# Performance work log

Measured on AMD Instinct MI355X. Metric: run time of the kernel, lower is better.

## Reference

```python
import jax, jax.numpy as jnp
import numpy as np

BATCH, T, C = 32, 600, 64
DEPTH = 2            # logsig depth 2 -> [increments, Levy areas]
N_SEGMENTS = 50
N_HIDDENS = 512
LOGSIG_CH = C + C * (C - 1) // 2   # 2080, Lyndon-word count at depth 2
IN_SIZE = C + LOGSIG_CH            # 2144 = logsig + start point


def _t_vec(nT, n_segments):
    # matches: [int(round(x)) for x in np.linspace(1, nT, n_segments+1)]
    return np.asarray([int(round(v)) for v in np.linspace(1, nT, n_segments + 1)])


def setup_inputs() -> dict:
    key = jax.random.key(0)
    k0, k1, k2, k3, k4 = jax.random.split(key, 5)
    x = jax.random.normal(k0, (BATCH, T, C), jnp.float32)
    s = 1.0 / np.sqrt(N_HIDDENS)
    w_ih = jax.random.uniform(k1, (4 * N_HIDDENS, IN_SIZE), jnp.float32, -s, s)
    w_hh = jax.random.uniform(k2, (4 * N_HIDDENS, N_HIDDENS), jnp.float32, -s, s)
    b_ih = jax.random.uniform(k3, (4 * N_HIDDENS,), jnp.float32, -s, s)
    b_hh = jax.random.uniform(k4, (4 * N_HIDDENS,), jnp.float32, -s, s)
    return {"x": x, "w_ih": w_ih, "w_hh": w_hh, "b_ih": b_ih, "b_hh": b_hh}


def _logsig_and_start(x):
    """Depth-2 segmented log-signature + segment start points.
    Returns (logsig (B,S,LOGSIG_CH), start (B,S,C))."""
    B, nT, c = x.shape
    tv = _t_vec(nT, N_SEGMENTS)
    starts = tv[:-1] - 1               # segment start frame indices
    ends = tv[1:] - 1                  # segment end frame indices
    # step s (between frames s and s+1) belongs to segment i iff tv[i]-1 <= s < tv[i+1]-1
    step_ids = jnp.asarray(np.searchsorted(tv[1:] - 1, np.arange(nT - 1), side='right'))
    dx = x[:, 1:] - x[:, :-1]                            # (B, T-1, C)
    # per-step outer product x_{t-} (X) dx_t, then segmented sum over steps
    prod = jnp.einsum('btc,btd->btcd', x[:, :-1], dx)    # (B, T-1, C, C)
    Q = jax.ops.segment_sum(jnp.moveaxis(prod, 1, 0), step_ids,
                            num_segments=N_SEGMENTS)      # (S, B, C, C)
    xa = x[:, starts]                                    # (B, S, C)
    xb = x[:, ends]
    inc = xb - xa                                        # level-1 logsig
    # shift origin to segment start: P = sum (X_rel (X) dX)
    P = jnp.moveaxis(Q, 0, 1) - jnp.einsum('bsc,bsd->bscd', xa, inc)
    A = 0.5 * (P - jnp.swapaxes(P, -1, -2))              # Levy area (antisym)
    iu, ju = np.triu_indices(c, 1)                       # Lyndon words (i,j), i<j, lex order
    logsig = jnp.concatenate([inc, A[:, :, iu, ju]], axis=-1)
    return logsig, xa


def _lstm(feats, w_ih, w_hh, b_ih, b_hh):
    B = feats.shape[0]
    H = N_HIDDENS
    gx = jnp.einsum('bsf,gf->bsg', feats, w_ih) + b_ih + b_hh  # (B,S,4H)

    def step(carry, g_t):
        h, cc = carry
        g = g_t + h @ w_hh.T
        i, f, gg, o = jnp.split(g, 4, axis=-1)
        i = jax.nn.sigmoid(i); f = jax.nn.sigmoid(f)
        gg = jnp.tanh(gg); o = jax.nn.sigmoid(o)
        cc = f * cc + i * gg
        h = o * jnp.tanh(cc)
        return (h, cc), h

    h0 = jnp.zeros((B, H), feats.dtype)
    (_, _), hs = jax.lax.scan(step, (h0, h0), jnp.moveaxis(gx, 1, 0))
    return jnp.moveaxis(hs, 0, 1)                        # (B, S, H)


def reference(x, w_ih, w_hh, b_ih, b_hh):
    logsig, x_sp = _logsig_and_start(x)
    feats = jnp.concatenate([logsig, x_sp], axis=-1)      # (B, S, IN_SIZE)
    return _lstm(feats, w_ih, w_hh, b_ih, b_hh)
```

## Files before the change

kernel.cpp:

```cpp
#include <hip/hip_runtime.h>
#include <math.h>

typedef _Float16 f16;
typedef _Float16 f16x8 __attribute__((ext_vector_type(8)));
typedef _Float16 f16x4 __attribute__((ext_vector_type(4)));
typedef float    f32x4 __attribute__((ext_vector_type(4)));

#define BATCH 32
#define TT    600
#define CC    64
#define SEG   50
#define HH    512
#define G4    2048
#define FF    2144
#define MM    1600
#define MP    1664
#define NPAIR 2016
#define CVB   512
#define WRK   208
#define SLOT16 16384

struct TV { int v[51]; };

__device__ __forceinline__ void async_copy16(char* lds, const char* g) {
  __builtin_amdgcn_global_load_lds(
      (const __attribute__((address_space(1))) unsigned int*)g,
      (__attribute__((address_space(3))) unsigned int*)lds, 16, 0, 0);
}

__device__ __forceinline__ float sigm(float x) { return 1.f / (1.f + __expf(-x)); }
__device__ __forceinline__ float tanh_(float x) {
  float ax = fabsf(x);
  float e  = __expf(2.f * ax);
  float t  = 1.f - 2.f / (e + 1.f);
  return x < 0.f ? -t : t;
}
__device__ __forceinline__ unsigned short f16_bits(f16 v) {
  union { f16 f; unsigned short u; } c; c.f = v; return c.u;
}
__device__ __forceinline__ unsigned int f32_bits(float v) {
  union { float f; unsigned int u; } c; c.f = v; return c.u;
}

__global__ void prep_kernel(const float* __restrict__ x, f16* __restrict__ fhi, TV tv,
                            const float4* __restrict__ w_ih, const float4* __restrict__ w_hh,
                            f16x4* __restrict__ w16, f16x4* __restrict__ whh16,
                            unsigned int* __restrict__ ready) {
  __shared__ float xs[13 * CC];
  int m   = blockIdx.x;
  int tid = threadIdx.x;

  if (m >= MP) {
    int cb   = m - MP;
    int gtid = cb * 256 + tid;
    int nth  = CVB * 256;
    for (int i = gtid; i < G4 * FF / 4; i += nth) {
      float4 v = w_ih[i];
      f16x4 o = {(f16)v.x, (f16)v.y, (f16)v.z, (f16)v.w};
      w16[i] = o;
    }
    for (int i = gtid; i < G4 * HH / 4; i += nth) {
      float4 v = w_hh[i];
      f16x4 o = {(f16)v.x, (f16)v.y, (f16)v.z, (f16)v.w};
      whh16[i] = o;
    }
    if (cb == 0)
      for (int i = tid; i < 544; i += 256) ready[i] = 0u;
    return;
  }

  f16* rhi = fhi + (size_t)m * FF;
  if (m >= MM) {
    unsigned int* a = (unsigned int*)rhi;
    for (int i = tid; i < FF / 2; i += 256) a[i] = 0u;
    return;
  }
  int bb = m & 31, ss = m >> 5;
  int t0 = tv.v[ss] - 1, t1 = tv.v[ss + 1] - 1;
  int len = t1 - t0;
  for (int i = tid; i < (len + 1) * CC; i += 256)
    xs[i] = x[(size_t)bb * TT * CC + (size_t)(t0 + (i >> 6)) * CC + (i & 63)];
  __syncthreads();

  if (tid < CC) {
    float xa  = xs[tid];
    float inc = xs[len * CC + tid] - xa;
    rhi[tid] = (f16)inc;
    rhi[2080 + tid] = (f16)xa;
  }

  int p0 = tid * 8;
  if (p0 < NPAIR) {
    int c = 0, rem = p0;
    while (rem >= 63 - c) { rem -= 63 - c; c++; }
    int d = c + 1 + rem;
    int cs[8], dd[8];
#pragma unroll
    for (int i = 0; i < 8; i++) {
      cs[i] = c; dd[i] = d;
      d++; if (d == 64) { c++; d = c + 1; }
    }
    float acc[8], xc[8], xd[8];
#pragma unroll
    for (int i = 0; i < 8; i++) { acc[i] = 0.f; xc[i] = xs[cs[i]]; xd[i] = xs[dd[i]]; }
    for (int t = 1; t <= len; t++) {
#pragma unroll
      for (int i = 0; i < 8; i++) {
        float nc = xs[t * CC + cs[i]], nd = xs[t * CC + dd[i]];
        acc[i] += xc[i] * (nd - xd[i]) - xd[i] * (nc - xc[i]);
        xc[i] = nc; xd[i] = nd;
      }
    }
#pragma unroll
    for (int i = 0; i < 8; i++) {
      int ci = cs[i], di = dd[i];
      float xac = xs[ci], xad = xs[di];
      float incc = xs[len * CC + ci] - xac, incd = xs[len * CC + di] - xad;
      float v = 0.5f * acc[i] - 0.5f * (xac * incd - xad * incc);
      rhi[64 + p0 + i] = (f16)v;
    }
  }
}

__global__ __launch_bounds__(256) void fused_kernel(
    const f16* __restrict__ fhi, const f16* __restrict__ w16,
    const float* __restrict__ bih, const float* __restrict__ bhh,
    const f16* __restrict__ whh16, float* __restrict__ gx,
    unsigned short* __restrict__ hbuf, unsigned int* __restrict__ ready,
    unsigned int* __restrict__ gxcnt, float* __restrict__ out) {
  __shared__ __align__(16) char smem[40960];
  int tid  = threadIdx.x;
  int lane = tid & 63;

  if (blockIdx.x >= 32) {
    int w  = blockIdx.x - 32;
    int wn = tid >> 6;
    char* ldsA = smem;
    char* ldsB = smem + 4096;
    int rowq = tid >> 2;
    int colq = (tid & 3) * 8;
    int ldst = tid * 16;
    int quad16 = (lane >> 4) * 16;
    int am = lane & 15;
    unsigned int* gxa = (unsigned int*)gx;

    for (int t = 0; t < 2; t++) {
      int id = w + t * WRK;
      int mt = id >> 4, nt = id & 15;
      int m0 = mt * 64, n0 = nt * 128;

      const f16* pa  = fhi + (size_t)(m0 + rowq) * FF + colq;
      const f16* pb0 = w16 + (size_t)(n0 + rowq) * FF + colq;
      const f16* pb1 = pb0 + (size_t)64 * FF;

      f32x4 zero4 = {0.f, 0.f, 0.f, 0.f};
      f32x4 acc[4][2];
#pragma unroll
      for (int i = 0; i < 4; i++) { acc[i][0] = zero4; acc[i][1] = zero4; }

      for (int kt = 0; kt < FF / 32; kt++) {
        int koff = kt * 32;
        async_copy16(ldsA + ldst,        (const char*)(pa + koff));
        async_copy16(ldsB + ldst,        (const char*)(pb0 + koff));
        async_copy16(ldsB + 4096 + ldst, (const char*)(pb1 + koff));
        __syncthreads();

        f16x8 bfr[2];
#pragma unroll
        for (int ni = 0; ni < 2; ni++)
          bfr[ni] = *(const f16x8*)(ldsB + (wn * 32 + ni * 16 + am) * 64 + quad16);
#pragma unroll
        for (int mi = 0; mi < 4; mi++) {
          f16x8 ah = *(const f16x8*)(ldsA + (mi * 16 + am) * 64 + quad16);
#pragma unroll
          for (int ni = 0; ni < 2; ni++)
            acc[mi][ni] = __builtin_amdgcn_mfma_f32_16x16x32_f16(ah, bfr[ni], acc[mi][ni], 0, 0, 0);
        }
        __syncthreads();
      }

#pragma unroll
      for (int ni = 0; ni < 2; ni++) {
        int ncol = n0 + wn * 32 + ni * 16 + (lane & 15);
        float bv = bih[ncol] + bhh[ncol];
#pragma unroll
        for (int mi = 0; mi < 4; mi++) {
          int mrow = m0 + mi * 16 + (lane >> 4) * 4;
#pragma unroll
          for (int r = 0; r < 4; r++)
            __hip_atomic_store(gxa + (size_t)(mrow + r) * G4 + ncol,
                               f32_bits(acc[mi][ni][r] + bv),
                               __ATOMIC_RELAXED, __HIP_MEMORY_SCOPE_AGENT);
        }
      }
      __syncthreads();
      if (tid == 0)
        __hip_atomic_fetch_add(&gxcnt[mt], 1u, __ATOMIC_RELAXED,
                               __HIP_MEMORY_SCOPE_AGENT);
    }
    return;
  }

  f16* hs = (f16*)smem;
  float* gb = (float*)(smem + 32768);

  int gate = tid >> 6;
  int u0   = blockIdx.x * 16;
  int wg   = blockIdx.x;

  f16x8 bf[16];
  {
    const f16* wrow = whh16 + (size_t)(gate * HH + u0 + (lane & 15)) * HH + (lane >> 4) * 8;
#pragma unroll
    for (int ks = 0; ks < 16; ks++) bf[ks] = *(const f16x8*)(wrow + ks * 32);
  }

  int b1 = tid >> 4;
  int ul = tid & 15;
  float cst0 = 0.f, cst1 = 0.f;
  int aq  = (lane >> 4);
  int am  = (lane & 15);
  int col = lane & 15;
  int rbase = (lane >> 4) * 4;

  for (int s = 0; s < SEG; s++) {
    if ((s & 1) == 0) {
      if (tid == 0) {
        while (__hip_atomic_load(&gxcnt[s >> 1], __ATOMIC_RELAXED,
                                 __HIP_MEMORY_SCOPE_AGENT) < 16u)
          __builtin_amdgcn_s_sleep(1);
      }
      __syncthreads();
    }

    float gxr0[4], gxr1[4];
#pragma unroll
    for (int r = 0; r < 4; r++) {
      int b = rbase + r;
      gxr0[r] = gx[(size_t)((s << 5) + b) * G4 + gate * HH + u0 + col];
      gxr1[r] = gx[(size_t)((s << 5) + b + 16) * G4 + gate * HH + u0 + col];
    }

    f32x4 acc0 = {0.f, 0.f, 0.f, 0.f};
    f32x4 acc1 = {0.f, 0.f, 0.f, 0.f};

    if (s > 0) {
      unsigned int tgt = (unsigned int)s;
      if (tid < 32) {
        while (__hip_atomic_load(&ready[tid * 16], __ATOMIC_RELAXED,
                                 __HIP_MEMORY_SCOPE_AGENT) < tgt)
          __builtin_amdgcn_s_sleep(1);
      }
      __syncthreads();

      const char* hrd = (const char*)(hbuf + (size_t)s * SLOT16);
#pragma unroll
      for (int c = 0; c < 8; c++)
        async_copy16((char*)hs + c * 4096 + tid * 16, hrd + c * 4096 + tid * 16);
      __syncthreads();

#pragma unroll
      for (int ks = 0; ks < 16; ks++) {
        f16x8 a0 = *(const f16x8*)((char*)hs + (((ks * 4 + aq) * 32) + am) * 16);
        f16x8 a1 = *(const f16x8*)((char*)hs + (((ks * 4 + aq) * 32) + 16 + am) * 16);
        acc0 = __builtin_amdgcn_mfma_f32_16x16x32_f16(a0, bf[ks], acc0, 0, 0, 0);
        acc1 = __builtin_amdgcn_mfma_f32_16x16x32_f16(a1, bf[ks], acc1, 0, 0, 0);
      }
    }

#pragma unroll
    for (int r = 0; r < 4; r++) {
      int b = rbase + r;
      gb[(gate * 32 + b) * 16 + col]      = acc0[r] + gxr0[r];
      gb[(gate * 32 + b + 16) * 16 + col] = acc1[r] + gxr1[r];
    }
    __syncthreads();

    unsigned short* hwr = hbuf + (size_t)(s + 1) * SLOT16;
    int k = u0 + ul;
    float h0, h1;
    {
      float i_ = sigm(gb[(0 * 32 + b1) * 16 + ul]), f_ = sigm(gb[(1 * 32 + b1) * 16 + ul]);
      float g_ = tanh_(gb[(2 * 32 + b1) * 16 + ul]), o_ = sigm(gb[(3 * 32 + b1) * 16 + ul]);
      cst0 = f_ * cst0 + i_ * g_;
      h0 = o_ * tanh_(cst0);
      out[(size_t)(b1 * SEG + s) * HH + k] = h0;
    }
    {
      int b2 = b1 + 16;
      float i_ = sigm(gb[(0 * 32 + b2) * 16 + ul]), f_ = sigm(gb[(1 * 32 + b2) * 16 + ul]);
      float g_ = tanh_(gb[(2 * 32 + b2) * 16 + ul]), o_ = sigm(gb[(3 * 32 + b2) * 16 + ul]);
      cst1 = f_ * cst1 + i_ * g_;
      h1 = o_ * tanh_(cst1);
      out[(size_t)(b2 * SEG + s) * HH + k] = h1;
    }

    if (s < SEG - 1) {
      __hip_atomic_store(hwr + ((k >> 3) * 32 + b1) * 8 + (k & 7),
                         f16_bits((f16)h0), __ATOMIC_RELAXED, __HIP_MEMORY_SCOPE_AGENT);
      __hip_atomic_store(hwr + ((k >> 3) * 32 + (b1 + 16)) * 8 + (k & 7),
                         f16_bits((f16)h1), __ATOMIC_RELAXED, __HIP_MEMORY_SCOPE_AGENT);
      __syncthreads();
      if (tid == 0)
        __hip_atomic_store(&ready[wg * 16], (unsigned int)(s + 1),
                           __ATOMIC_RELAXED, __HIP_MEMORY_SCOPE_AGENT);
    }
  }
}

extern "C" void kernel_launch(void* const* d_in, const int* in_sizes, int n_in,
                              void* d_out, int out_size, void* d_ws, size_t ws_size,
                              hipStream_t stream) {
  const float* x    = (const float*)d_in[0];
  const float* w_ih = (const float*)d_in[1];
  const float* w_hh = (const float*)d_in[2];
  const float* b_ih = (const float*)d_in[3];
  const float* b_hh = (const float*)d_in[4];
  float* out = (float*)d_out;

  char* ws = (char*)d_ws;
  f16*   fhi   = (f16*)(ws + 0);
  f16*   w16   = (f16*)(ws + 7135232);
  f16*   whh16 = (f16*)(ws + 15921152);
  float* gx    = (float*)(ws + 18018304);
  unsigned short* hbuf  = (unsigned short*)(ws + 31649792);
  unsigned int*   ready = (unsigned int*)(ws + 33288192);

  TV tv;
  double step = 599.0 / 50.0;
  for (int i = 0; i <= 50; i++) {
    double v = (double)i * step + 1.0;
    tv.v[i] = (int)nearbyint(v);
  }
  tv.v[50] = 600;

  unsigned int* gxcnt = ready + 512;

  prep_kernel<<<dim3(MP + CVB), dim3(256), 0, stream>>>(
      x, fhi, tv, (const float4*)w_ih, (const float4*)w_hh,
      (f16x4*)w16, (f16x4*)whh16, ready);

  fused_kernel<<<dim3(32 + WRK), dim3(256), 0, stream>>>(
      fhi, w16, b_ih, b_hh, whh16, gx, hbuf, ready, gxcnt, out);
}
```

Before: 264.8 us.

## Pack LSTM recurrence flags, poll per wave, prefetch two steps of gx

Ready flags drop their 16-word padding and sit in consecutive words. Each wave polls them itself, lane-distributed, instead of tid<32 spinning followed by a block barrier. The gx values for two timesteps are loaded after each gxcnt wait, and the elementwise cell update now gives each thread two adjacent units of one batch row, so hidden state is stored as packed 32-bit f16 pairs and outputs as float2. The aim is fewer barriers and narrow atomic stores on the serial recurrence path. The cost is packed flags that may share cache lines and more register pressure.

Result: slower. 274.7 us (+3.8%).

```diff
diff --git a/kernel.cpp b/kernel.cpp
--- a/kernel.cpp
+++ b/kernel.cpp
@@ -35,8 +35,8 @@
   float t  = 1.f - 2.f / (e + 1.f);
   return x < 0.f ? -t : t;
 }
-__device__ __forceinline__ unsigned short f16_bits(f16 v) {
-  union { f16 f; unsigned short u; } c; c.f = v; return c.u;
+__device__ __forceinline__ unsigned int f16_bits(f16 v) {
+  union { f16 f; unsigned short u; } c; c.f = v; return (unsigned int)c.u;
 }
 __device__ __forceinline__ unsigned int f32_bits(float v) {
   union { float f; unsigned int u; } c; c.f = v; return c.u;
@@ -65,7 +65,7 @@
       whh16[i] = o;
     }
     if (cb == 0)
-      for (int i = tid; i < 544; i += 256) ready[i] = 0u;
+      if (tid < 64) ready[tid] = 0u;
     return;
   }
 
@@ -205,6 +205,7 @@
   float* gb = (float*)(smem + 32768);
 
   int gate = tid >> 6;
+  int wave = gate;
   int u0   = blockIdx.x * 16;
   int wg   = blockIdx.x;
 
@@ -215,44 +216,40 @@
     for (int ks = 0; ks < 16; ks++) bf[ks] = *(const f16x8*)(wrow + ks * 32);
   }
 
-  int b1 = tid >> 4;
-  int ul = tid & 15;
-  float cst0 = 0.f, cst1 = 0.f;
   int aq  = (lane >> 4);
   int am  = (lane & 15);
   int col = lane & 15;
   int rbase = (lane >> 4) * 4;
+  int ub = tid >> 3;
+  int uj = tid & 7;
+  int koct = (u0 >> 3) + (uj >> 2);
+  float cstA = 0.f, cstB = 0.f;
+  int pollp = ((lane & 7) << 2) | wave;
+
+  float gxA[2][4], gxB[2][4];
 
   for (int s = 0; s < SEG; s++) {
-    if ((s & 1) == 0) {
-      if (tid == 0) {
-        while (__hip_atomic_load(&gxcnt[s >> 1], __ATOMIC_RELAXED,
-                                 __HIP_MEMORY_SCOPE_AGENT) < 16u)
-          __builtin_amdgcn_s_sleep(1);
-      }
-      __syncthreads();
-    }
-
-    float gxr0[4], gxr1[4];
-#pragma unroll
-    for (int r = 0; r < 4; r++) {
-      int b = rbase + r;
-      gxr0[r] = gx[(size_t)((s << 5) + b) * G4 + gate * HH + u0 + col];
-      gxr1[r] = gx[(size_t)((s << 5) + b + 16) * G4 + gate * HH + u0 + col];
+    if (!(s & 1)) {
+      while (__hip_atomic_load(&gxcnt[s >> 1], __ATOMIC_RELAXED,
+                               __HIP_MEMORY_SCOPE_AGENT) < 16u)
+        __builtin_amdgcn_s_sleep(1);
+#pragma unroll
+      for (int h = 0; h < 2; h++)
+#pragma unroll
+        for (int r = 0; r < 4; r++) {
+          int b = rbase + r;
+          gxA[h][r] = gx[(size_t)(((s + h) << 5) + b) * G4 + gate * HH + u0 + col];
+          gxB[h][r] = gx[(size_t)(((s + h) << 5) + b + 16) * G4 + gate * HH + u0 + col];
+        }
     }
 
     f32x4 acc0 = {0.f, 0.f, 0.f, 0.f};
     f32x4 acc1 = {0.f, 0.f, 0.f, 0.f};
 
     if (s > 0) {
-      unsigned int tgt = (unsigned int)s;
-      if (tid < 32) {
-        while (__hip_atomic_load(&ready[tid * 16], __ATOMIC_RELAXED,
-                                 __HIP_MEMORY_SCOPE_AGENT) < tgt)
-          __builtin_amdgcn_s_sleep(1);
-      }
-      __syncthreads();
-
+      while (__hip_atomic_load(&ready[pollp], __ATOMIC_RELAXED,
+                               __HIP_MEMORY_SCOPE_AGENT) < (unsigned int)s)
+        __builtin_amdgcn_s_sleep(1);
       const char* hrd = (const char*)(hbuf + (size_t)s * SLOT16);
 #pragma unroll
       for (int c = 0; c < 8; c++)
@@ -268,43 +265,36 @@
       }
     }
 
+    int hsel = s & 1;
 #pragma unroll
     for (int r = 0; r < 4; r++) {
       int b = rbase + r;
-      gb[(gate * 32 + b) * 16 + col]      = acc0[r] + gxr0[r];
-      gb[(gate * 32 + b + 16) * 16 + col] = acc1[r] + gxr1[r];
+      gb[(gate * 32 + b) * 16 + col]      = acc0[r] + gxA[hsel][r];
+      gb[(gate * 32 + b + 16) * 16 + col] = acc1[r] + gxB[hsel][r];
     }
     __syncthreads();
 
-    unsigned short* hwr = hbuf + (size_t)(s + 1) * SLOT16;
-    int k = u0 + ul;
-    float h0, h1;
-    {
-      float i_ = sigm(gb[(0 * 32 + b1) * 16 + ul]), f_ = sigm(gb[(1 * 32 + b1) * 16 + ul]);
-      float g_ = tanh_(gb[(2 * 32 + b1) * 16 + ul]), o_ = sigm(gb[(3 * 32 + b1) * 16 + ul]);
-      cst0 = f_ * cst0 + i_ * g_;
-      h0 = o_ * tanh_(cst0);
-      out[(size_t)(b1 * SEG + s) * HH + k] = h0;
-    }
-    {
-      int b2 = b1 + 16;
-      float i_ = sigm(gb[(0 * 32 + b2) * 16 + ul]), f_ = sigm(gb[(1 * 32 + b2) * 16 + ul]);
-      float g_ = tanh_(gb[(2 * 32 + b2) * 16 + ul]), o_ = sigm(gb[(3 * 32 + b2) * 16 + ul]);
-      cst1 = f_ * cst1 + i_ * g_;
-      h1 = o_ * tanh_(cst1);
-      out[(size_t)(b2 * SEG + s) * HH + k] = h1;
-    }
+    float2 gi = *(float2*)&gb[(0 * 32 + ub) * 16 + 2 * uj];
+    float2 gf = *(float2*)&gb[(1 * 32 + ub) * 16 + 2 * uj];
+    float2 gg = *(float2*)&gb[(2 * 32 + ub) * 16 + 2 * uj];
+    float2 go = *(float2*)&gb[(3 * 32 + ub) * 16 + 2 * uj];
+    cstA = sigm(gf.x) * cstA + sigm(gi.x) * tanh_(gg.x);
+    float hA = sigm(go.x) * tanh_(cstA);
+    cstB = sigm(gf.y) * cstB + sigm(gi.y) * tanh_(gg.y);
+    float hB = sigm(go.y) * tanh_(cstB);
 
     if (s < SEG - 1) {
-      __hip_atomic_store(hwr + ((k >> 3) * 32 + b1) * 8 + (k & 7),
-                         f16_bits((f16)h0), __ATOMIC_RELAXED, __HIP_MEMORY_SCOPE_AGENT);
-      __hip_atomic_store(hwr + ((k >> 3) * 32 + (b1 + 16)) * 8 + (k & 7),
-                         f16_bits((f16)h1), __ATOMIC_RELAXED, __HIP_MEMORY_SCOPE_AGENT);
+      unsigned int hp = f16_bits((f16)hA) | (f16_bits((f16)hB) << 16);
+      unsigned int* hwr = (unsigned int*)hbuf + (size_t)(s + 1) * (SLOT16 / 2);
+      __hip_atomic_store(hwr + (koct * 32 + ub) * 4 + (uj & 3), hp,
+                         __ATOMIC_RELAXED, __HIP_MEMORY_SCOPE_AGENT);
       __syncthreads();
       if (tid == 0)
-        __hip_atomic_store(&ready[wg * 16], (unsigned int)(s + 1),
+        __hip_atomic_store(&ready[wg], (unsigned int)(s + 1),
                            __ATOMIC_RELAXED, __HIP_MEMORY_SCOPE_AGENT);
     }
+    float2 ho = {hA, hB};
+    *(float2*)(out + (size_t)(ub * SEG + s) * HH + u0 + 2 * uj) = ho;
   }
 }
 
@@ -334,7 +324,7 @@
   }
   tv.v[50] = 600;
 
-  unsigned int* gxcnt = ready + 512;
+  unsigned int* gxcnt = ready + 32;
 
   prep_kernel<<<dim3(MP + CVB), dim3(256), 0, stream>>>(
       x, fhi, tv, (const float4*)w_ih, (const float4*)w_hh,
```
